# Kernel tuning notes

Measured on AMD Instinct MI355X. Metric: run time of the kernel, lower is better.

Reference implementation:

```python
import jax, jax.numpy as jnp
import numpy as np

T, H, I, E = 2048, 2880, 2880, 8
TOP_K = 4
ALPHA = 1.702   # hidden_act_alpha
LIMIT = 7.0     # swiglu_limit
BETA = 1.0      # swiglu_beta


def setup_inputs() -> dict:
    key = jax.random.key(0)
    ks = jax.random.split(key, 10)
    s = 0.02
    return {
        "hidden_states": jax.random.normal(ks[0], (T, H), dtype=jnp.float32),
        "w_router": jax.random.normal(ks[1], (E, H), dtype=jnp.float32) * s,
        "b_router": jax.random.normal(ks[2], (E,), dtype=jnp.float32) * s,
        "w_gate": jax.random.normal(ks[3], (E, I, H), dtype=jnp.float32) * s,
        "b_gate": jax.random.normal(ks[4], (E, I), dtype=jnp.float32) * s,
        "w_up": jax.random.normal(ks[5], (E, I, H), dtype=jnp.float32) * s,
        "b_up": jax.random.normal(ks[6], (E, I), dtype=jnp.float32) * s,
        "w2": jax.random.normal(ks[7], (E, H, I), dtype=jnp.float32) * s,
        "b2": jax.random.normal(ks[8], (E, H), dtype=jnp.float32) * s,
        "num_global_tokens": T,
        "max_num_tokens_per_gpu": T,
    }


def reference(hidden_states, w_router, b_router, w_gate, b_gate, w_up, b_up,
              w2, b2, num_global_tokens, max_num_tokens_per_gpu):
    x = hidden_states  # [T, H]
    # ---- router + custom routing_function: topk then softmax over topk logits (fp32)
    router_logits = x @ w_router.T + b_router                 # [T, E]
    topk_vals, topk_idx = jax.lax.top_k(router_logits, TOP_K)  # [T, K]
    expert_weights = jax.nn.softmax(topk_vals.astype(jnp.float32), axis=-1)  # [T, K]
    # combine weights per expert: [T, E], nonzero only for the top-k experts
    tok = jnp.arange(x.shape[0])[:, None]
    combine = jnp.zeros((x.shape[0], E), dtype=jnp.float32).at[tok, topk_idx].add(expert_weights)
    # ---- experts: gpt-oss swiglu with clamp limits and +beta on up branch
    g = jnp.einsum('th,eih->tei', x, w_gate) + b_gate[None]   # [T, E, I]
    u = jnp.einsum('th,eih->tei', x, w_up) + b_up[None]       # [T, E, I]
    g = jnp.minimum(g, LIMIT)
    u = jnp.clip(u, -LIMIT, LIMIT)
    act = (u + BETA) * (g * jax.nn.sigmoid(ALPHA * g))        # [T, E, I]
    y = jnp.einsum('tei,ehi->teh', act, w2) + b2[None]        # [T, E, H]
    out = jnp.einsum('teh,te->th', y, combine)                # [T, H]
    return out.astype(x.dtype)
```

## Files before the change

### kernel.cpp

```cpp
#include <hip/hip_runtime.h>
#include <cstdint>
#include <cstddef>

#define T_TOK 2048
#define HD    2880
#define ID    2880
#define NE    8
#define TOPK  4
#define ALPHA 1.702f
#define LIMIT 7.0f

typedef __attribute__((ext_vector_type(8))) short short8;
typedef __attribute__((ext_vector_type(4))) float floatx4;

__device__ __forceinline__ ushort f32_bf16(float f) {
    union { float f; uint32_t u; } c; c.f = f;
    uint32_t u = c.u;
    uint32_t r = (u + 0x7FFFu + ((u >> 16) & 1u)) >> 16;
    return (ushort)r;
}

__device__ __forceinline__ void gload_lds16(const void* g, void* l) {
    __builtin_amdgcn_global_load_lds(
        (const __attribute__((address_space(1))) void*)g,
        (__attribute__((address_space(3))) void*)l,
        16, 0, 0);
}

__global__ __launch_bounds__(256) void cvt_x_kernel(const float* __restrict__ x,
                                                    ushort* __restrict__ xb) {
    int i = (blockIdx.x * 256 + threadIdx.x) * 4;
    float4 v = *(const float4*)(x + i);
    ushort4 o;
    o.x = f32_bf16(v.x); o.y = f32_bf16(v.y);
    o.z = f32_bf16(v.z); o.w = f32_bf16(v.w);
    *(ushort4*)(xb + i) = o;
}

__global__ __launch_bounds__(256) void cvt_w_kernel(const float* __restrict__ w,
                                                    ushort* __restrict__ wb, int n4) {
    int stride = gridDim.x * 256;
    for (int i = blockIdx.x * 256 + threadIdx.x; i < n4; i += stride) {
        float4 v = *(const float4*)(w + (size_t)i * 4);
        ushort4 o;
        o.x = f32_bf16(v.x); o.y = f32_bf16(v.y);
        o.z = f32_bf16(v.z); o.w = f32_bf16(v.w);
        *(ushort4*)(wb + (size_t)i * 4) = o;
    }
}

__global__ __launch_bounds__(256) void router_kernel(
    const float* __restrict__ x, const float* __restrict__ wr,
    const float* __restrict__ br, int* __restrict__ cnt,
    int* __restrict__ tok_list, float* __restrict__ wgt_list) {
    const int t = blockIdx.x, tid = threadIdx.x;
    __shared__ float sx[HD];
    __shared__ float sred[NE][4];
    for (int h = tid; h < HD; h += 256) sx[h] = x[(size_t)t * HD + h];
    __syncthreads();
    float p[NE];
#pragma unroll
    for (int e = 0; e < NE; e++) p[e] = 0.f;
    for (int h = tid; h < HD; h += 256) {
        float xv = sx[h];
#pragma unroll
        for (int e = 0; e < NE; e++) p[e] = fmaf(xv, wr[e * HD + h], p[e]);
    }
#pragma unroll
    for (int e = 0; e < NE; e++) {
#pragma unroll
        for (int off = 32; off > 0; off >>= 1) p[e] += __shfl_down(p[e], off, 64);
    }
    if ((tid & 63) == 0) {
#pragma unroll
        for (int e = 0; e < NE; e++) sred[e][tid >> 6] = p[e];
    }
    __syncthreads();
    if (tid == 0) {
        float lg[NE];
#pragma unroll
        for (int e = 0; e < NE; e++)
            lg[e] = sred[e][0] + sred[e][1] + sred[e][2] + sred[e][3] + br[e];
        int idx[TOPK]; float val[TOPK];
        unsigned used = 0;
#pragma unroll
        for (int k = 0; k < TOPK; k++) {
            int best = -1; float bv = -1e30f;
#pragma unroll
            for (int e = 0; e < NE; e++) {
                if (!((used >> e) & 1u) && lg[e] > bv) { bv = lg[e]; best = e; }
            }
            used |= 1u << best; idx[k] = best; val[k] = bv;
        }
        float m = val[0];
        float ex[TOPK], s = 0.f;
#pragma unroll
        for (int k = 0; k < TOPK; k++) { ex[k] = __expf(val[k] - m); s += ex[k]; }
        float inv = 1.f / s;
#pragma unroll
        for (int k = 0; k < TOPK; k++) {
            int e = idx[k];
            int pos = atomicAdd(&cnt[e], 1);
            tok_list[e * T_TOK + pos] = t;
            wgt_list[e * T_TOK + pos] = ex[k] * inv;
        }
    }
}

__global__ void offsets_kernel(const int* __restrict__ cnt, int* __restrict__ ofs) {
    if (threadIdx.x == 0 && blockIdx.x == 0) {
        int s = 0;
        for (int e = 0; e < NE; e++) { ofs[e] = s; s += cnt[e]; }
    }
}


__global__ __launch_bounds__(256, 2) void expert_gu2_kernel(
    const ushort* __restrict__ xb, const ushort* __restrict__ wgb,
    const float* __restrict__ bg, const ushort* __restrict__ wub,
    const float* __restrict__ bu, const int* __restrict__ cnt,
    const int* __restrict__ ofs, const int* __restrict__ tok_list,
    ushort* __restrict__ act) {
    const int e = blockIdx.z;
    const int n_e = cnt[e];
    const int mBase = blockIdx.y * 128;
    if (mBase >= n_e) return;
    const int nBase = blockIdx.x * 128;
    const int tid = threadIdx.x;

    __shared__ __attribute__((aligned(16))) ushort sA[128 * 32];
    __shared__ __attribute__((aligned(16))) ushort sBg[128 * 32];
    __shared__ __attribute__((aligned(16))) ushort sBu[128 * 32];
    __shared__ int sTok[128];

    if (tid < 128) {
        int slot = mBase + tid;
        sTok[tid] = tok_list[e * T_TOK + (slot < n_e ? slot : 0)];
    }
    __syncthreads();

    const ushort* wgE = wgb + (size_t)e * (size_t)ID * HD;
    const ushort* wuE = wub + (size_t)e * (size_t)ID * HD;
    const ushort* aSrc[2];
    const ushort* gSrc[2];
    const ushort* uSrc[2];
#pragma unroll
    for (int i = 0; i < 2; i++) {
        int lin = i * 256 + tid;
        int ar = lin >> 2, ac = lin & 3;
        aSrc[i] = xb + (size_t)sTok[ar] * HD + ac * 8;
        int n = nBase + ar; if (n >= ID) n = ID - 1;
        gSrc[i] = wgE + (size_t)n * HD + ac * 8;
        uSrc[i] = wuE + (size_t)n * HD + ac * 8;
    }

    const int wave = tid >> 6, lane = tid & 63;
    const int wm = (wave >> 1) * 64, wn = (wave & 1) * 64;
    const int ln = lane & 15, quad = lane >> 4;

    floatx4 accG[4][4], accU[4][4];
#pragma unroll
    for (int mi = 0; mi < 4; mi++)
#pragma unroll
        for (int ni = 0; ni < 4; ni++) {
            accG[mi][ni] = (floatx4){0.f, 0.f, 0.f, 0.f};
            accU[mi][ni] = (floatx4){0.f, 0.f, 0.f, 0.f};
        }

    for (int k0 = 0; k0 < HD; k0 += 32) {
#pragma unroll
        for (int i = 0; i < 2; i++) {
            int lin = i * 256 + tid;
            gload_lds16(aSrc[i] + k0, &sA[lin * 8]);
            gload_lds16(gSrc[i] + k0, &sBg[lin * 8]);
            gload_lds16(uSrc[i] + k0, &sBu[lin * 8]);
        }
        __syncthreads();

        short8 af[4], bgf[4], buf_[4];
#pragma unroll
        for (int mi = 0; mi < 4; mi++)
            af[mi] = *(const short8*)&sA[(wm + mi * 16 + ln) * 32 + quad * 8];
#pragma unroll
        for (int ni = 0; ni < 4; ni++) {
            bgf[ni] = *(const short8*)&sBg[(wn + ni * 16 + ln) * 32 + quad * 8];
            buf_[ni] = *(const short8*)&sBu[(wn + ni * 16 + ln) * 32 + quad * 8];
        }
#pragma unroll
        for (int mi = 0; mi < 4; mi++)
#pragma unroll
            for (int ni = 0; ni < 4; ni++) {
                accG[mi][ni] = __builtin_amdgcn_mfma_f32_16x16x32_bf16(
                    af[mi], bgf[ni], accG[mi][ni], 0, 0, 0);
                accU[mi][ni] = __builtin_amdgcn_mfma_f32_16x16x32_bf16(
                    af[mi], buf_[ni], accU[mi][ni], 0, 0, 0);
            }
        __syncthreads();
    }

    const int row0 = ofs[e] + mBase;
#pragma unroll
    for (int mi = 0; mi < 4; mi++) {
#pragma unroll
        for (int r = 0; r < 4; r++) {
            int ml = wm + mi * 16 + quad * 4 + r;
            if (mBase + ml >= n_e) continue;
#pragma unroll
            for (int ni = 0; ni < 4; ni++) {
                int n = nBase + wn + ni * 16 + ln;
                if (n < ID) {
                    float g = accG[mi][ni][r] + bg[e * ID + n];
                    float u = accU[mi][ni][r] + bu[e * ID + n];
                    g = fminf(g, LIMIT);
                    u = fminf(fmaxf(u, -LIMIT), LIMIT);
                    float sg = 1.0f / (1.0f + __expf(-ALPHA * g));
                    float a = (u + 1.0f) * (g * sg);
                    act[(size_t)(row0 + ml) * ID + n] = f32_bf16(a);
                }
            }
        }
    }
}

__global__ __launch_bounds__(256, 2) void expert_down2_kernel(
    const ushort* __restrict__ act, const ushort* __restrict__ w2b,
    const float* __restrict__ b2, const int* __restrict__ cnt,
    const int* __restrict__ ofs, const int* __restrict__ tok_list,
    const float* __restrict__ wgt_list, float* __restrict__ out) {
    const int e = blockIdx.z;
    const int n_e = cnt[e];
    const int mBase = blockIdx.y * 128;
    if (mBase >= n_e) return;
    const int nBase = blockIdx.x * 128;
    const int tid = threadIdx.x;

    __shared__ __attribute__((aligned(16))) ushort sA[128 * 32];
    __shared__ __attribute__((aligned(16))) ushort sB[128 * 32];
    __shared__ int sTok[128];
    __shared__ float sWgt[128];

    if (tid < 128) {
        int slot = mBase + tid;
        int cs = (slot < n_e) ? slot : 0;
        sTok[tid] = tok_list[e * T_TOK + cs];
        sWgt[tid] = wgt_list[e * T_TOK + cs];
    }
    __syncthreads();

    const int row0 = ofs[e] + mBase;
    const ushort* w2E = w2b + (size_t)e * (size_t)HD * ID;
    const ushort* aSrc[2];
    const ushort* bSrc[2];
#pragma unroll
    for (int i = 0; i < 2; i++) {
        int lin = i * 256 + tid;
        int ar = lin >> 2, ac = lin & 3;
        int rr = (mBase + ar < n_e) ? ar : 0;
        aSrc[i] = act + (size_t)(row0 + rr) * ID + ac * 8;
        int n = nBase + ar; if (n >= HD) n = HD - 1;
        bSrc[i] = w2E + (size_t)n * ID + ac * 8;
    }

    const int wave = tid >> 6, lane = tid & 63;
    const int wm = (wave >> 1) * 64, wn = (wave & 1) * 64;
    const int ln = lane & 15, quad = lane >> 4;

    floatx4 acc[4][4];
#pragma unroll
    for (int mi = 0; mi < 4; mi++)
#pragma unroll
        for (int ni = 0; ni < 4; ni++) acc[mi][ni] = (floatx4){0.f, 0.f, 0.f, 0.f};

    for (int k0 = 0; k0 < ID; k0 += 32) {
#pragma unroll
        for (int i = 0; i < 2; i++) {
            int lin = i * 256 + tid;
            gload_lds16(aSrc[i] + k0, &sA[lin * 8]);
            gload_lds16(bSrc[i] + k0, &sB[lin * 8]);
        }
        __syncthreads();

        short8 af[4], bf[4];
#pragma unroll
        for (int mi = 0; mi < 4; mi++)
            af[mi] = *(const short8*)&sA[(wm + mi * 16 + ln) * 32 + quad * 8];
#pragma unroll
        for (int ni = 0; ni < 4; ni++)
            bf[ni] = *(const short8*)&sB[(wn + ni * 16 + ln) * 32 + quad * 8];
#pragma unroll
        for (int mi = 0; mi < 4; mi++)
#pragma unroll
            for (int ni = 0; ni < 4; ni++)
                acc[mi][ni] = __builtin_amdgcn_mfma_f32_16x16x32_bf16(
                    af[mi], bf[ni], acc[mi][ni], 0, 0, 0);
        __syncthreads();
    }

#pragma unroll
    for (int mi = 0; mi < 4; mi++) {
#pragma unroll
        for (int r = 0; r < 4; r++) {
            int ml = wm + mi * 16 + quad * 4 + r;
            if (mBase + ml >= n_e) continue;
            int token = sTok[ml];
            float wgt = sWgt[ml];
#pragma unroll
            for (int ni = 0; ni < 4; ni++) {
                int n = nBase + wn + ni * 16 + ln;
                if (n < HD) {
                    float v = (acc[mi][ni][r] + b2[e * HD + n]) * wgt;
                    atomicAdd(&out[(size_t)token * HD + n], v);
                }
            }
        }
    }
}

#define LDS_S 40
__global__ __launch_bounds__(256, 2) void expert_gu_kernel(
    const ushort* __restrict__ xb, const float* __restrict__ wg,
    const float* __restrict__ bg, const float* __restrict__ wu,
    const float* __restrict__ bu, const int* __restrict__ cnt,
    const int* __restrict__ ofs, const int* __restrict__ tok_list,
    ushort* __restrict__ act) {
    const int e = blockIdx.z;
    const int n_e = cnt[e];
    const int mBase = blockIdx.y * 128;
    if (mBase >= n_e) return;
    const int nBase = blockIdx.x * 128;
    const int tid = threadIdx.x;

    __shared__ ushort sA[128 * LDS_S];
    __shared__ ushort sBg[128 * LDS_S];
    __shared__ ushort sBu[128 * LDS_S];
    __shared__ int sTok[128];

    if (tid < 128) {
        int slot = mBase + tid;
        sTok[tid] = tok_list[e * T_TOK + (slot < n_e ? slot : 0)];
    }
    __syncthreads();

    const int wave = tid >> 6, lane = tid & 63;
    const int wm = (wave >> 1) * 64, wn = (wave & 1) * 64;
    const int ln = lane & 15, quad = lane >> 4;

    floatx4 accG[4][4], accU[4][4];
#pragma unroll
    for (int mi = 0; mi < 4; mi++)
#pragma unroll
        for (int ni = 0; ni < 4; ni++) {
            accG[mi][ni] = (floatx4){0.f, 0.f, 0.f, 0.f};
            accU[mi][ni] = (floatx4){0.f, 0.f, 0.f, 0.f};
        }

    const float* wgE = wg + (size_t)e * ID * HD;
    const float* wuE = wu + (size_t)e * ID * HD;

    for (int k0 = 0; k0 < HD; k0 += 32) {
#pragma unroll
        for (int r = 0; r < 2; r++) {
            int lin = r * 256 + tid;
            int ar = lin >> 2, ac = lin & 3;
            uint4 v = *(const uint4*)(xb + (size_t)sTok[ar] * HD + k0 + ac * 8);
            *(uint4*)&sA[ar * LDS_S + ac * 8] = v;
        }
#pragma unroll
        for (int r = 0; r < 4; r++) {
            int c = r * 256 + tid;
            int brow = c >> 3, bc = c & 7;
            int n = nBase + brow; if (n >= ID) n = ID - 1;
            float4 g4 = *(const float4*)(wgE + (size_t)n * HD + k0 + bc * 4);
            float4 u4 = *(const float4*)(wuE + (size_t)n * HD + k0 + bc * 4);
            ushort4 gg, uu;
            gg.x = f32_bf16(g4.x); gg.y = f32_bf16(g4.y);
            gg.z = f32_bf16(g4.z); gg.w = f32_bf16(g4.w);
            uu.x = f32_bf16(u4.x); uu.y = f32_bf16(u4.y);
            uu.z = f32_bf16(u4.z); uu.w = f32_bf16(u4.w);
            *(ushort4*)&sBg[brow * LDS_S + bc * 4] = gg;
            *(ushort4*)&sBu[brow * LDS_S + bc * 4] = uu;
        }
        __syncthreads();
        short8 af[4], bgf[4], buf_[4];
#pragma unroll
        for (int mi = 0; mi < 4; mi++)
            af[mi] = *(const short8*)&sA[(wm + mi * 16 + ln) * LDS_S + quad * 8];
#pragma unroll
        for (int ni = 0; ni < 4; ni++) {
            bgf[ni] = *(const short8*)&sBg[(wn + ni * 16 + ln) * LDS_S + quad * 8];
            buf_[ni] = *(const short8*)&sBu[(wn + ni * 16 + ln) * LDS_S + quad * 8];
        }
#pragma unroll
        for (int mi = 0; mi < 4; mi++)
#pragma unroll
            for (int ni = 0; ni < 4; ni++) {
                accG[mi][ni] = __builtin_amdgcn_mfma_f32_16x16x32_bf16(
                    af[mi], bgf[ni], accG[mi][ni], 0, 0, 0);
                accU[mi][ni] = __builtin_amdgcn_mfma_f32_16x16x32_bf16(
                    af[mi], buf_[ni], accU[mi][ni], 0, 0, 0);
            }
        __syncthreads();
    }

    const int row0 = ofs[e] + mBase;
#pragma unroll
    for (int mi = 0; mi < 4; mi++) {
#pragma unroll
        for (int r = 0; r < 4; r++) {
            int ml = wm + mi * 16 + quad * 4 + r;
            if (mBase + ml >= n_e) continue;
#pragma unroll
            for (int ni = 0; ni < 4; ni++) {
                int n = nBase + wn + ni * 16 + ln;
                if (n < ID) {
                    float g = accG[mi][ni][r] + bg[e * ID + n];
                    float u = accU[mi][ni][r] + bu[e * ID + n];
                    g = fminf(g, LIMIT);
                    u = fminf(fmaxf(u, -LIMIT), LIMIT);
                    float sg = 1.0f / (1.0f + __expf(-ALPHA * g));
                    float a = (u + 1.0f) * (g * sg);
                    act[(size_t)(row0 + ml) * ID + n] = f32_bf16(a);
                }
            }
        }
    }
}

__global__ __launch_bounds__(256, 2) void expert_down_kernel(
    const ushort* __restrict__ act, const float* __restrict__ w2,
    const float* __restrict__ b2, const int* __restrict__ cnt,
    const int* __restrict__ ofs, const int* __restrict__ tok_list,
    const float* __restrict__ wgt_list, float* __restrict__ out) {
    const int e = blockIdx.z;
    const int n_e = cnt[e];
    const int mBase = blockIdx.y * 128;
    if (mBase >= n_e) return;
    const int nBase = blockIdx.x * 128;
    const int tid = threadIdx.x;

    __shared__ ushort sA[128 * LDS_S];
    __shared__ ushort sB[128 * LDS_S];
    __shared__ int sTok[128];
    __shared__ float sWgt[128];

    if (tid < 128) {
        int slot = mBase + tid;
        int cs = (slot < n_e) ? slot : 0;
        sTok[tid] = tok_list[e * T_TOK + cs];
        sWgt[tid] = wgt_list[e * T_TOK + cs];
    }
    __syncthreads();

    const int wave = tid >> 6, lane = tid & 63;
    const int wm = (wave >> 1) * 64, wn = (wave & 1) * 64;
    const int ln = lane & 15, quad = lane >> 4;
    const int row0 = ofs[e] + mBase;

    floatx4 acc[4][4];
#pragma unroll
    for (int mi = 0; mi < 4; mi++)
#pragma unroll
        for (int ni = 0; ni < 4; ni++) acc[mi][ni] = (floatx4){0.f, 0.f, 0.f, 0.f};

    const float* w2E = w2 + (size_t)e * HD * ID;

    for (int k0 = 0; k0 < ID; k0 += 32) {
#pragma unroll
        for (int r = 0; r < 2; r++) {
            int lin = r * 256 + tid;
            int ar = lin >> 2, ac = lin & 3;
            int rr = (mBase + ar < n_e) ? ar : 0;
            uint4 v = *(const uint4*)(act + (size_t)(row0 + rr) * ID + k0 + ac * 8);
            *(uint4*)&sA[ar * LDS_S + ac * 8] = v;
        }
#pragma unroll
        for (int r = 0; r < 4; r++) {
            int c = r * 256 + tid;
            int brow = c >> 3, bc = c & 7;
            int n = nBase + brow; if (n >= HD) n = HD - 1;
            float4 b4 = *(const float4*)(w2E + (size_t)n * ID + k0 + bc * 4);
            ushort4 bb;
            bb.x = f32_bf16(b4.x); bb.y = f32_bf16(b4.y);
            bb.z = f32_bf16(b4.z); bb.w = f32_bf16(b4.w);
            *(ushort4*)&sB[brow * LDS_S + bc * 4] = bb;
        }
        __syncthreads();
        short8 af[4], bf[4];
#pragma unroll
        for (int mi = 0; mi < 4; mi++)
            af[mi] = *(const short8*)&sA[(wm + mi * 16 + ln) * LDS_S + quad * 8];
#pragma unroll
        for (int ni = 0; ni < 4; ni++)
            bf[ni] = *(const short8*)&sB[(wn + ni * 16 + ln) * LDS_S + quad * 8];
#pragma unroll
        for (int mi = 0; mi < 4; mi++)
#pragma unroll
            for (int ni = 0; ni < 4; ni++)
                acc[mi][ni] = __builtin_amdgcn_mfma_f32_16x16x32_bf16(
                    af[mi], bf[ni], acc[mi][ni], 0, 0, 0);
        __syncthreads();
    }

#pragma unroll
    for (int mi = 0; mi < 4; mi++) {
#pragma unroll
        for (int r = 0; r < 4; r++) {
            int ml = wm + mi * 16 + quad * 4 + r;
            if (mBase + ml >= n_e) continue;
            int token = sTok[ml];
            float wgt = sWgt[ml];
#pragma unroll
            for (int ni = 0; ni < 4; ni++) {
                int n = nBase + wn + ni * 16 + ln;
                if (n < HD) {
                    float v = (acc[mi][ni][r] + b2[e * HD + n]) * wgt;
                    atomicAdd(&out[(size_t)token * HD + n], v);
                }
            }
        }
    }
}

extern "C" void kernel_launch(void* const* d_in, const int* in_sizes, int n_in,
                              void* d_out, int out_size, void* d_ws, size_t ws_size,
                              hipStream_t stream) {
    const float* x  = (const float*)d_in[0];
    const float* wr = (const float*)d_in[1];
    const float* br = (const float*)d_in[2];
    const float* wg = (const float*)d_in[3];
    const float* bg = (const float*)d_in[4];
    const float* wu = (const float*)d_in[5];
    const float* bu = (const float*)d_in[6];
    const float* w2 = (const float*)d_in[7];
    const float* b2 = (const float*)d_in[8];
    float* out = (float*)d_out;

    char* ws = (char*)d_ws;
    int*    cnt      = (int*)ws;
    int*    ofs      = (int*)(ws + 256);
    int*    tok_list = (int*)(ws + 512);
    float*  wgt_list = (float*)(ws + 512 + 65536);
    ushort* xb       = (ushort*)(ws + 131584);
    ushort* act      = (ushort*)(ws + 131584 + 11796480);
    const size_t W_ELEMS = (size_t)NE * ID * HD;
    ushort* wgb = (ushort*)(ws + 59113984);
    ushort* wub = (ushort*)(ws + 59113984 + 132710400);
    ushort* w2b = (ushort*)(ws + 59113984 + 2ull * 132710400);
    const size_t NEED = 59113984ull + 3ull * 132710400ull;

    hipMemsetAsync(out, 0, (size_t)T_TOK * HD * sizeof(float), stream);
    hipMemsetAsync(cnt, 0, NE * sizeof(int), stream);

    cvt_x_kernel<<<(T_TOK * HD) / 4 / 256, 256, 0, stream>>>(x, xb);
    router_kernel<<<T_TOK, 256, 0, stream>>>(x, wr, br, cnt, tok_list, wgt_list);
    offsets_kernel<<<1, 64, 0, stream>>>(cnt, ofs);

    if (ws_size >= NEED) {
        const int n4 = (int)(W_ELEMS / 4);
        cvt_w_kernel<<<8192, 256, 0, stream>>>(wg, wgb, n4);
        cvt_w_kernel<<<8192, 256, 0, stream>>>(wu, wub, n4);
        cvt_w_kernel<<<8192, 256, 0, stream>>>(w2, w2b, n4);

        dim3 g1((ID + 127) / 128, T_TOK / 128, NE);
        expert_gu2_kernel<<<g1, 256, 0, stream>>>(xb, wgb, bg, wub, bu, cnt, ofs,
                                                  tok_list, act);
        dim3 g2((HD + 127) / 128, T_TOK / 128, NE);
        expert_down2_kernel<<<g2, 256, 0, stream>>>(act, w2b, b2, cnt, ofs, tok_list,
                                                    wgt_list, out);
    } else {
        dim3 g1((ID + 127) / 128, T_TOK / 128, NE);
        expert_gu_kernel<<<g1, 256, 0, stream>>>(xb, wg, bg, wu, bu, cnt, ofs,
                                                 tok_list, act);
        dim3 g2((HD + 127) / 128, T_TOK / 128, NE);
        expert_down_kernel<<<g2, 256, 0, stream>>>(act, w2, b2, cnt, ofs, tok_list,
                                                   wgt_list, out);
    }
}
```

Before: 1.723 ms.

## Replace atomic scatter in down projection with per-slot buffer and combine kernel

Adds a non-atomic down-projection kernel that writes weighted per-slot expert outputs to a workspace buffer, plus a combine kernel that sums each token's top-k rows through a token-to-slot map recorded by the router. This is meant to remove the contended float atomics on the output. It also flattens the grouped-GEMM grids to 1D with a swizzled work decode, so blocks sharing an expert and column tile are spread across compute units. The cost is an extra ~94 MB fp32 buffer that is written and then read back, and one more kernel launch; the new path only runs if the workspace is large enough.

```diff
diff --git a/kernel.cpp b/kernel.cpp
--- a/kernel.cpp
+++ b/kernel.cpp
@@ -10,6 +10,10 @@
 #define ALPHA 1.702f
 #define LIMIT 7.0f
 
+#define NXB 23
+#define NYB 16
+#define NWG (NXB * NYB * NE)
+
 typedef __attribute__((ext_vector_type(8))) short short8;
 typedef __attribute__((ext_vector_type(4))) float floatx4;
 
@@ -25,6 +29,14 @@
         (const __attribute__((address_space(1))) void*)g,
         (__attribute__((address_space(3))) void*)l,
         16, 0, 0);
+}
+
+__device__ __forceinline__ void decode_work(int b, int& e, int& xq, int& y) {
+    int w = (b & 7) * (NWG >> 3) + (b >> 3);
+    y = w & 15;
+    int rest = w >> 4;
+    e = rest & 7;
+    xq = rest >> 3;
 }
 
 __global__ __launch_bounds__(256) void cvt_x_kernel(const float* __restrict__ x,
@@ -52,7 +64,8 @@
 __global__ __launch_bounds__(256) void router_kernel(
     const float* __restrict__ x, const float* __restrict__ wr,
     const float* __restrict__ br, int* __restrict__ cnt,
-    int* __restrict__ tok_list, float* __restrict__ wgt_list) {
+    int* __restrict__ tok_list, float* __restrict__ wgt_list,
+    int* __restrict__ t2s) {
     const int t = blockIdx.x, tid = threadIdx.x;
     __shared__ float sx[HD];
     __shared__ float sred[NE][4];
@@ -103,6 +116,7 @@
             int pos = atomicAdd(&cnt[e], 1);
             tok_list[e * T_TOK + pos] = t;
             wgt_list[e * T_TOK + pos] = ex[k] * inv;
+            if (t2s) t2s[t * TOPK + k] = e * T_TOK + pos;
         }
     }
 }
@@ -121,11 +135,12 @@
     const float* __restrict__ bu, const int* __restrict__ cnt,
     const int* __restrict__ ofs, const int* __restrict__ tok_list,
     ushort* __restrict__ act) {
-    const int e = blockIdx.z;
+    int e, xq, y;
+    decode_work(blockIdx.x, e, xq, y);
     const int n_e = cnt[e];
-    const int mBase = blockIdx.y * 128;
+    const int mBase = y * 128;
     if (mBase >= n_e) return;
-    const int nBase = blockIdx.x * 128;
+    const int nBase = xq * 128;
     const int tid = threadIdx.x;
 
     __shared__ __attribute__((aligned(16))) ushort sA[128 * 32];
@@ -222,16 +237,130 @@
     }
 }
 
+__global__ __launch_bounds__(256, 2) void expert_down2_na_kernel(
+    const ushort* __restrict__ act, const ushort* __restrict__ w2b,
+    const float* __restrict__ b2, const int* __restrict__ cnt,
+    const int* __restrict__ ofs, const float* __restrict__ wgt_list,
+    float* __restrict__ yws) {
+    int e, xq, y;
+    decode_work(blockIdx.x, e, xq, y);
+    const int n_e = cnt[e];
+    const int mBase = y * 128;
+    if (mBase >= n_e) return;
+    const int nBase = xq * 128;
+    const int tid = threadIdx.x;
+
+    __shared__ __attribute__((aligned(16))) ushort sA[128 * 32];
+    __shared__ __attribute__((aligned(16))) ushort sB[128 * 32];
+    __shared__ float sWgt[128];
+
+    if (tid < 128) {
+        int slot = mBase + tid;
+        int cs = (slot < n_e) ? slot : 0;
+        sWgt[tid] = wgt_list[e * T_TOK + cs];
+    }
+    __syncthreads();
+
+    const int row0 = ofs[e] + mBase;
+    const ushort* w2E = w2b + (size_t)e * (size_t)HD * ID;
+    const ushort* aSrc[2];
+    const ushort* bSrc[2];
+#pragma unroll
+    for (int i = 0; i < 2; i++) {
+        int lin = i * 256 + tid;
+        int ar = lin >> 2, ac = lin & 3;
+        int rr = (mBase + ar < n_e) ? ar : 0;
+        aSrc[i] = act + (size_t)(row0 + rr) * ID + ac * 8;
+        int n = nBase + ar; if (n >= HD) n = HD - 1;
+        bSrc[i] = w2E + (size_t)n * ID + ac * 8;
+    }
+
+    const int wave = tid >> 6, lane = tid & 63;
+    const int wm = (wave >> 1) * 64, wn = (wave & 1) * 64;
+    const int ln = lane & 15, quad = lane >> 4;
+
+    floatx4 acc[4][4];
+#pragma unroll
+    for (int mi = 0; mi < 4; mi++)
+#pragma unroll
+        for (int ni = 0; ni < 4; ni++) acc[mi][ni] = (floatx4){0.f, 0.f, 0.f, 0.f};
+
+    for (int k0 = 0; k0 < ID; k0 += 32) {
+#pragma unroll
+        for (int i = 0; i < 2; i++) {
+            int lin = i * 256 + tid;
+            gload_lds16(aSrc[i] + k0, &sA[lin * 8]);
+            gload_lds16(bSrc[i] + k0, &sB[lin * 8]);
+        }
+        __syncthreads();
+
+        short8 af[4], bf[4];
+#pragma unroll
+        for (int mi = 0; mi < 4; mi++)
+            af[mi] = *(const short8*)&sA[(wm + mi * 16 + ln) * 32 + quad * 8];
+#pragma unroll
+        for (int ni = 0; ni < 4; ni++)
+            bf[ni] = *(const short8*)&sB[(wn + ni * 16 + ln) * 32 + quad * 8];
+#pragma unroll
+        for (int mi = 0; mi < 4; mi++)
+#pragma unroll
+            for (int ni = 0; ni < 4; ni++)
+                acc[mi][ni] = __builtin_amdgcn_mfma_f32_16x16x32_bf16(
+                    af[mi], bf[ni], acc[mi][ni], 0, 0, 0);
+        __syncthreads();
+    }
+
+#pragma unroll
+    for (int mi = 0; mi < 4; mi++) {
+#pragma unroll
+        for (int r = 0; r < 4; r++) {
+            int ml = wm + mi * 16 + quad * 4 + r;
+            if (mBase + ml >= n_e) continue;
+            float wgt = sWgt[ml];
+#pragma unroll
+            for (int ni = 0; ni < 4; ni++) {
+                int n = nBase + wn + ni * 16 + ln;
+                if (n < HD) {
+                    yws[(size_t)(row0 + ml) * HD + n] =
+                        (acc[mi][ni][r] + b2[e * HD + n]) * wgt;
+                }
+            }
+        }
+    }
+}
+
+__global__ __launch_bounds__(256) void combine_kernel(
+    const float* __restrict__ yws, const int* __restrict__ t2s,
+    const int* __restrict__ ofs, float* __restrict__ out) {
+    const int t = blockIdx.x, tid = threadIdx.x;
+    int rows[TOPK];
+#pragma unroll
+    for (int k = 0; k < TOPK; k++) {
+        int slot = t2s[t * TOPK + k];
+        rows[k] = ofs[slot >> 11] + (slot & (T_TOK - 1));
+    }
+    for (int i = tid; i < HD / 4; i += 256) {
+        float4 s = *(const float4*)(yws + (size_t)rows[0] * HD + i * 4);
+#pragma unroll
+        for (int k = 1; k < TOPK; k++) {
+            float4 v = *(const float4*)(yws + (size_t)rows[k] * HD + i * 4);
+            s.x += v.x; s.y += v.y; s.z += v.z; s.w += v.w;
+        }
+        *(float4*)(out + (size_t)t * HD + i * 4) = s;
+    }
+}
+
 __global__ __launch_bounds__(256, 2) void expert_down2_kernel(
     const ushort* __restrict__ act, const ushort* __restrict__ w2b,
     const float* __restrict__ b2, const int* __restrict__ cnt,
     const int* __restrict__ ofs, const int* __restrict__ tok_list,
     const float* __restrict__ wgt_list, float* __restrict__ out) {
-    const int e = blockIdx.z;
+    int e, xq, y;
+    decode_work(blockIdx.x, e, xq, y);
     const int n_e = cnt[e];
-    const int mBase = blockIdx.y * 128;
+    const int mBase = y * 128;
     if (mBase >= n_e) return;
-    const int nBase = blockIdx.x * 128;
+    const int nBase = xq * 128;
     const int tid = threadIdx.x;
 
     __shared__ __attribute__((aligned(16))) ushort sA[128 * 32];
@@ -547,26 +676,37 @@
     ushort* wub = (ushort*)(ws + 59113984 + 132710400);
     ushort* w2b = (ushort*)(ws + 59113984 + 2ull * 132710400);
     const size_t NEED = 59113984ull + 3ull * 132710400ull;
+    int*   t2s = (int*)(ws + NEED);
+    float* yws = (float*)(ws + NEED + 32768);
+    const size_t NEED3 = NEED + 32768ull + 94371840ull;
+
+    const bool bf16_path = (ws_size >= NEED);
+    const bool na_path   = (ws_size >= NEED3);
 
     hipMemsetAsync(out, 0, (size_t)T_TOK * HD * sizeof(float), stream);
     hipMemsetAsync(cnt, 0, NE * sizeof(int), stream);
 
     cvt_x_kernel<<<(T_TOK * HD) / 4 / 256, 256, 0, stream>>>(x, xb);
-    router_kernel<<<T_TOK, 256, 0, stream>>>(x, wr, br, cnt, tok_list, wgt_list);
+    router_kernel<<<T_TOK, 256, 0, stream>>>(x, wr, br, cnt, tok_list, wgt_list,
+                                             na_path ? t2s : nullptr);
     offsets_kernel<<<1, 64, 0, stream>>>(cnt, ofs);
 
-    if (ws_size >= NEED) {
+    if (bf16_path) {
         const int n4 = (int)(W_ELEMS / 4);
         cvt_w_kernel<<<8192, 256, 0, stream>>>(wg, wgb, n4);
         cvt_w_kernel<<<8192, 256, 0, stream>>>(wu, wub, n4);
         cvt_w_kernel<<<8192, 256, 0, stream>>>(w2, w2b, n4);
 
-        dim3 g1((ID + 127) / 128, T_TOK / 128, NE);
-        expert_gu2_kernel<<<g1, 256, 0, stream>>>(xb, wgb, bg, wub, bu, cnt, ofs,
-                                                  tok_list, act);
-        dim3 g2((HD + 127) / 128, T_TOK / 128, NE);
-        expert_down2_kernel<<<g2, 256, 0, stream>>>(act, w2b, b2, cnt, ofs, tok_list,
-                                                    wgt_list, out);
+        expert_gu2_kernel<<<NWG, 256, 0, stream>>>(xb, wgb, bg, wub, bu, cnt, ofs,
+                                                   tok_list, act);
+        if (na_path) {
+            expert_down2_na_kernel<<<NWG, 256, 0, stream>>>(act, w2b, b2, cnt, ofs,
+                                                            wgt_list, yws);
+            combine_kernel<<<T_TOK, 256, 0, stream>>>(yws, t2s, ofs, out);
+        } else {
+            expert_down2_kernel<<<NWG, 256, 0, stream>>>(act, w2b, b2, cnt, ofs,
+                                                         tok_list, wgt_list, out);
+        }
     } else {
         dim3 g1((ID + 127) / 128, T_TOK / 128, NE);
         expert_gu_kernel<<<g1, 256, 0, stream>>>(xb, wg, bg, wu, bu, cnt, ofs,
```

After: 1.599 ms. -7.2%, faster.
